# Kernel optimization log

Hardware: AMD Instinct MI355X
Metric: run time of the kernel (lower is better)

The kernel has to match this reference:

```python
import math
import jax, jax.numpy as jnp
import numpy as np

FACTOR = 2  # init kwarg of AutoCorrelation


def setup_inputs() -> dict:
    key0 = jax.random.key(0)
    kq, kk, kv = jax.random.split(key0, 3)
    B, H, L, D = 8, 8, 2048, 64
    return {
        "query": jax.random.normal(kq, (B, H, L, D), dtype=jnp.float32),
        "key": jax.random.normal(kk, (B, H, L, D), dtype=jnp.float32),
        "value": jax.random.normal(kv, (B, H, L, D), dtype=jnp.float32),
    }


def reference(query, key, value):
    # Inference (eval-mode) path of AutoCorrelation.forward.
    B, H, L, D = query.shape
    L_KV = key.shape[2]
    # _pad_or_truncate_key_value: match key/value length to query length
    if L > L_KV:
        pad = [(0, 0), (0, 0), (0, L - L_KV), (0, 0)]
        key = jnp.pad(key, pad)
        value = jnp.pad(value, pad)
    else:
        key = key[:, :, :L, :]
        value = value[:, :, :L, :]

    # _period_based_dependency: circular cross-correlation via FFT
    qf = jnp.fft.rfft(jnp.swapaxes(query, -2, -1), axis=-1)   # (B,H,D,L//2+1) complex
    kf = jnp.fft.rfft(jnp.swapaxes(key, -2, -1), axis=-1)
    corr = jnp.fft.irfft(qf * jnp.conj(kf), n=L, axis=-1)     # (B,H,D,L)

    # _time_delay_aggregation (eval branch: per-batch topk delays)
    mean_corr = corr.mean(axis=(1, 2))                         # (B,L)
    num_delays = min(FACTOR * math.ceil(math.log(L)), L)
    w, delay_idx = jax.lax.top_k(mean_corr, num_delays)       # (B,k)
    w = jax.nn.softmax(w, axis=-1)

    ar = jnp.arange(L)

    def body(ctx, inp):
        d, wk = inp  # (B,), (B,)
        idx = (ar[None, :] + d[:, None]) % L                   # (B,L) — circular shift == gather from doubled value
        gathered = jnp.take_along_axis(
            value, jnp.broadcast_to(idx[:, None, :, None], value.shape), axis=2
        )                                                      # (B,H,L,D)
        return ctx + wk[:, None, None, None] * gathered, None

    ctx0 = jnp.zeros_like(value)
    context, _ = jax.lax.scan(body, ctx0, (delay_idx.T, w.T))
    return context
```

## Files before the change

### kernel.cpp

```cpp
#include <hip/hip_runtime.h>

static constexpr int LSEQ = 2048;
static constexpr int NB   = 8;
static constexpr int NH   = 8;
static constexpr int ND   = 64;
static constexpr int NDEL = 16;

static constexpr size_t WS_P_OFF     = 0;
static constexpr size_t WS_S_OFF     = 8388608;
static constexpr size_t WS_W_OFF     = 8519680;
static constexpr size_t WS_DELAY_OFF = 8520192;

__device__ __forceinline__ int SW2(int j) { return j ^ ((j >> 4) & 15); }

__global__ __launch_bounds__(256) void fft_corr(const float* __restrict__ q,
                                                const float* __restrict__ k,
                                                float2* __restrict__ P) {
    __shared__ float2 z[4][LSEQ];
    __shared__ float2 tw[680];

    const int tid = threadIdx.x;
    const int bi  = blockIdx.x;
    const int xcd = bi & 7;
    const int sl  = bi >> 3;
    const int bh  = xcd * 8 + (sl >> 3);
    const int grp = sl & 7;
    const int b   = bh >> 3;
    const int h   = bh & 7;
    const size_t base = (size_t)bh * LSEQ * ND + (size_t)(grp * 8);

    for (int i = tid; i < 680; i += 256) {
        int idx, M;
        if (i < 512)      { idx = i;       M = 2048; }
        else if (i < 640) { idx = i - 512; M = 512; }
        else if (i < 672) { idx = i - 640; M = 128; }
        else              { idx = i - 672; M = 32; }
        float sn, cs;
        __sincosf(-6.28318530717958647692f * (float)idx / (float)M, &sn, &cs);
        tw[i] = make_float2(cs, sn);
    }

    float4 qa[8], ka[8];
    #pragma unroll
    for (int u = 0; u < 8; ++u) {
        const size_t r = base + (size_t)(tid + 256 * u) * ND;
        qa[u] = *(const float4*)(q + r);
        ka[u] = *(const float4*)(k + r);
    }
    #pragma unroll
    for (int u = 0; u < 8; ++u) {
        const int t = tid + 256 * u;
        #pragma unroll
        for (int c = 0; c < 4; ++c)
            z[c][SW2(t)] = make_float2((&qa[u].x)[c], (&ka[u].x)[c]);
    }
    float4 qb[8], kb[8];
    #pragma unroll
    for (int u = 0; u < 8; ++u) {
        const size_t r = base + (size_t)(tid + 256 * u) * ND + 4;
        qb[u] = *(const float4*)(q + r);
        kb[u] = *(const float4*)(k + r);
    }

    float accR[8], accI[8];
    #pragma unroll
    for (int u = 0; u < 8; ++u) { accR[u] = 0.f; accI[u] = 0.f; }

    const int lane = tid & 63;
    const int wch  = tid >> 6;
    const float RH = 0.70710678118654752440f;

    for (int round = 0; round < 2; ++round) {
        __syncthreads();

        const int tb[4] = {0, 512, 640, 672};
        #pragma unroll
        for (int st = 0; st < 4; ++st) {
            const int lq = 9 - 2 * st;
            const int qq = 1 << lq;
            const float2* twb = &tw[tb[st]];
            #pragma unroll
            for (int u = 0; u < 8; ++u) {
                const int j  = lane + (u << 6);
                const int kk = j & (qq - 1);
                const int i0 = ((j >> lq) << (lq + 2)) | kk;
                const float2 x0 = z[wch][SW2(i0)];
                const float2 x1 = z[wch][SW2(i0 + qq)];
                const float2 x2 = z[wch][SW2(i0 + 2 * qq)];
                const float2 x3 = z[wch][SW2(i0 + 3 * qq)];
                const float2 w1 = twb[kk];
                const float cs = w1.x, sn = w1.y;
                const float c2 = cs * cs - sn * sn, s2 = 2.f * cs * sn;
                const float Ar = x0.x + x2.x, Ai = x0.y + x2.y;
                const float B0r = x0.x - x2.x, B0i = x0.y - x2.y;
                const float Cr = x1.x + x3.x, Ci = x1.y + x3.y;
                const float D0r = x1.x - x3.x, D0i = x1.y - x3.y;
                z[wch][SW2(i0)] = make_float2(Ar + Cr, Ai + Ci);
                const float T1r = Ar - Cr, T1i = Ai - Ci;
                z[wch][SW2(i0 + qq)] =
                    make_float2(T1r * c2 - T1i * s2, T1r * s2 + T1i * c2);
                const float Br = B0r * cs - B0i * sn, Bi = B0r * sn + B0i * cs;
                const float Dr = D0r * sn + D0i * cs, Di = D0i * sn - D0r * cs;
                z[wch][SW2(i0 + 2 * qq)] = make_float2(Br + Dr, Bi + Di);
                const float T3r = Br - Dr, T3i = Bi - Di;
                z[wch][SW2(i0 + 3 * qq)] =
                    make_float2(T3r * c2 - T3i * s2, T3r * s2 + T3i * c2);
            }
            __syncthreads();
        }

        #pragma unroll
        for (int c4 = 0; c4 < 4; ++c4) {
            const int pb = tid << 3;
            float2 e[8];
            #pragma unroll
            for (int c = 0; c < 8; ++c) e[c] = z[c4][SW2(pb | c)];
            float ur[4], ui[4], vr[4], vi[4];
            ur[0] = e[0].x + e[4].x; ui[0] = e[0].y + e[4].y;
            vr[0] = e[0].x - e[4].x; vi[0] = e[0].y - e[4].y;
            { const float a = e[1].x - e[5].x, bq = e[1].y - e[5].y;
              ur[1] = e[1].x + e[5].x; ui[1] = e[1].y + e[5].y;
              vr[1] = RH * (a + bq); vi[1] = RH * (bq - a); }
            { const float a = e[2].x - e[6].x, bq = e[2].y - e[6].y;
              ur[2] = e[2].x + e[6].x; ui[2] = e[2].y + e[6].y;
              vr[2] = bq; vi[2] = -a; }
            { const float a = e[3].x - e[7].x, bq = e[3].y - e[7].y;
              ur[3] = e[3].x + e[7].x; ui[3] = e[3].y + e[7].y;
              vr[3] = RH * (bq - a); vi[3] = -RH * (a + bq); }
            {
                const float a0r = ur[0] + ur[2], a0i = ui[0] + ui[2];
                const float a2r = ur[0] - ur[2], a2i = ui[0] - ui[2];
                const float a1r = ur[1] + ur[3], a1i = ui[1] + ui[3];
                const float a3r = ui[1] - ui[3], a3i = -(ur[1] - ur[3]);
                z[c4][SW2(pb | 0)] = make_float2(a0r + a1r, a0i + a1i);
                z[c4][SW2(pb | 1)] = make_float2(a0r - a1r, a0i - a1i);
                z[c4][SW2(pb | 2)] = make_float2(a2r + a3r, a2i + a3i);
                z[c4][SW2(pb | 3)] = make_float2(a2r - a3r, a2i - a3i);
            }
            {
                const float a0r = vr[0] + vr[2], a0i = vi[0] + vi[2];
                const float a2r = vr[0] - vr[2], a2i = vi[0] - vi[2];
                const float a1r = vr[1] + vr[3], a1i = vi[1] + vi[3];
                const float a3r = vi[1] - vi[3], a3i = -(vr[1] - vr[3]);
                z[c4][SW2(pb | 4)] = make_float2(a0r + a1r, a0i + a1i);
                z[c4][SW2(pb | 5)] = make_float2(a0r - a1r, a0i - a1i);
                z[c4][SW2(pb | 6)] = make_float2(a2r + a3r, a2i + a3i);
                z[c4][SW2(pb | 7)] = make_float2(a2r - a3r, a2i - a3i);
            }
        }
        __syncthreads();

        #pragma unroll
        for (int u = 0; u < 8; ++u) {
            const int fb = wch * 8 + u;
            const int f  = fb | (lane << 5);
            const int m  = (2048 - f) & 2047;
            const int p  = (int)(__brev((unsigned)f) >> 21);
            const int pm = (int)(__brev((unsigned)m) >> 21);
            float sr = 0.f, si = 0.f;
            #pragma unroll
            for (int c = 0; c < 4; ++c) {
                const float2 Zf = z[c][SW2(p)];
                const float2 Zm = z[c][SW2(pm)];
                const float qr = 0.5f * (Zf.x + Zm.x), qi = 0.5f * (Zf.y - Zm.y);
                const float kr = 0.5f * (Zf.y + Zm.y), ki = 0.5f * (Zm.x - Zf.x);
                sr += qr * kr + qi * ki;
                si += qi * kr - qr * ki;
            }
            accR[u] += sr; accI[u] += si;
        }

        if (round == 0) {
            __syncthreads();
            #pragma unroll
            for (int u = 0; u < 8; ++u) {
                const int t = tid + 256 * u;
                #pragma unroll
                for (int c = 0; c < 4; ++c)
                    z[c][SW2(t)] = make_float2((&qb[u].x)[c], (&kb[u].x)[c]);
            }
        }
    }

    const int part = h * 8 + grp;
    float2* Pp = P + (size_t)part * (NB * 2048) + (size_t)b * 2048;
    #pragma unroll
    for (int u = 0; u < 8; ++u) {
        const int f = (wch * 8 + u) | (lane << 5);
        const int p = (int)(__brev((unsigned)f) >> 21);
        Pp[p] = make_float2(accR[u], accI[u]);
    }
}

__global__ __launch_bounds__(256) void reduce_S(const float2* __restrict__ P,
                                                float2* __restrict__ S) {
    const int g = blockIdx.x * 256 + threadIdx.x;
    float accx = 0.f, accy = 0.f;
    #pragma unroll 8
    for (int part = 0; part < 64; ++part) {
        const float2 v = P[(size_t)part * (NB * 2048) + g];
        accx += v.x; accy += v.y;
    }
    S[g] = make_float2(accx, accy);
}

__global__ __launch_bounds__(1024) void ifft_topk(const float2* __restrict__ S,
                                                  float* __restrict__ wout,
                                                  int* __restrict__ dout) {
    const int b = blockIdx.x, tid = threadIdx.x;
    __shared__ float2 y[LSEQ];
    __shared__ float  mc[LSEQ];
    __shared__ float  pv[16];
    __shared__ int    pi[16];
    __shared__ float  topv[NDEL];
    __shared__ int    topi[NDEL];

    y[tid]        = S[b * 2048 + tid];
    y[tid + 1024] = S[b * 2048 + tid + 1024];
    __syncthreads();

    for (int M = 2; M <= LSEQ; M <<= 1) {
        const int   half = M >> 1;
        const float w0   = 6.28318530717958647692f / (float)M;
        const int   kk = tid & (half - 1), i0 = 2 * tid - kk, i1 = i0 + half;
        const float2 a = y[i0], bb = y[i1];
        float sn, cs;
        __sincosf(w0 * (float)kk, &sn, &cs);
        const float tx = bb.x * cs - bb.y * sn, ty = bb.x * sn + bb.y * cs;
        y[i0] = make_float2(a.x + tx, a.y + ty);
        y[i1] = make_float2(a.x - tx, a.y - ty);
        __syncthreads();
    }

    const float scale = 1.0f / ((float)LSEQ * (float)(NH * ND));
    mc[tid]        = y[tid].x * scale;
    mc[tid + 1024] = y[tid + 1024].x * scale;
    __syncthreads();

    const int lane = tid & 63, wv = tid >> 6;
    for (int it = 0; it < NDEL; ++it) {
        const float v0 = mc[tid], v1 = mc[tid + 1024];
        float bv; int bix;
        if (v1 > v0) { bv = v1; bix = tid + 1024; } else { bv = v0; bix = tid; }
        #pragma unroll
        for (int off = 32; off; off >>= 1) {
            const float ov = __shfl_xor(bv, off);
            const int   oi = __shfl_xor(bix, off);
            if (ov > bv || (ov == bv && oi < bix)) { bv = ov; bix = oi; }
        }
        if (lane == 0) { pv[wv] = bv; pi[wv] = bix; }
        __syncthreads();
        if (tid < 64) {
            float v = (tid < 16) ? pv[tid] : -3e38f;
            int  ii = (tid < 16) ? pi[tid] : 0;
            #pragma unroll
            for (int off = 8; off; off >>= 1) {
                const float ov = __shfl_xor(v, off);
                const int   oi = __shfl_xor(ii, off);
                if (ov > v || (ov == v && oi < ii)) { v = ov; ii = oi; }
            }
            if (tid == 0) { topv[it] = v; topi[it] = ii; mc[ii] = -3e38f; }
        }
        __syncthreads();
    }

    if (tid == 0) {
        const float m = topv[0];
        float e[NDEL], sum = 0.f;
        for (int t2 = 0; t2 < NDEL; ++t2) { e[t2] = __expf(topv[t2] - m); sum += e[t2]; }
        const float inv = 1.0f / sum;
        for (int t2 = 0; t2 < NDEL; ++t2) {
            wout[b * NDEL + t2] = e[t2] * inv;
            dout[b * NDEL + t2] = topi[t2];
        }
    }
}

__global__ __launch_bounds__(256) void gather_out(const float* __restrict__ v,
                                                  const float* __restrict__ w,
                                                  const int* __restrict__ delay,
                                                  float* __restrict__ out) {
    const int bi  = blockIdx.x;
    const int xcd = bi & 7;
    const int s   = bi >> 3;
    const int bh  = xcd * 8 + (s >> 7);
    const int bt  = s & 127;
    const int b   = bh >> 3;
    const int tid = threadIdx.x;

    __shared__ float sw_[NDEL];
    __shared__ int   sd_[NDEL];
    if (tid < NDEL) {
        sw_[tid] = w[b * NDEL + tid];
        sd_[tid] = delay[b * NDEL + tid];
    }
    __syncthreads();

    const float* vb = v + (size_t)bh * LSEQ * ND;
    float*       ob = out + (size_t)bh * LSEQ * ND;

    const int row = tid >> 4;
    const int col = (tid & 15) * 4;
    const int t   = bt * 16 + row;

    float4 acc = make_float4(0.f, 0.f, 0.f, 0.f);
    #pragma unroll
    for (int kk = 0; kk < NDEL; ++kk) {
        const int r = (t + sd_[kk]) & (LSEQ - 1);
        const float4 vv = *(const float4*)(vb + (size_t)r * ND + col);
        const float wv = sw_[kk];
        acc.x += wv * vv.x; acc.y += wv * vv.y;
        acc.z += wv * vv.z; acc.w += wv * vv.w;
    }
    *(float4*)(ob + (size_t)t * ND + col) = acc;
}

extern "C" void kernel_launch(void* const* d_in, const int* in_sizes, int n_in,
                              void* d_out, int out_size, void* d_ws, size_t ws_size,
                              hipStream_t stream) {
    const float* q = (const float*)d_in[0];
    const float* k = (const float*)d_in[1];
    const float* v = (const float*)d_in[2];
    float* out = (float*)d_out;

    float2* P     = (float2*)((char*)d_ws + WS_P_OFF);
    float2* S     = (float2*)((char*)d_ws + WS_S_OFF);
    float*  w     = (float*)((char*)d_ws + WS_W_OFF);
    int*    delay = (int*)((char*)d_ws + WS_DELAY_OFF);

    fft_corr<<<dim3(512), dim3(256), 0, stream>>>(q, k, P);
    reduce_S<<<dim3(64), dim3(256), 0, stream>>>(P, S);
    ifft_topk<<<dim3(NB), dim3(1024), 0, stream>>>(S, w, delay);
    gather_out<<<dim3(NB * NH * 128), dim3(256), 0, stream>>>(v, w, delay, out);
}
```

Before: 226.9 us.

## Restructure FFT as radix-8 Stockham with register twiddles and fuse reduction into ifft

Replaces the four-column shared-memory radix-4 FFT with a single-column radix-8x8x8x4 decomposition that holds twiddles in registers and keeps the first pass in registers from global loads. Hermitian symmetry is used so each thread computes only half the spectrum bins and writes the conjugate mirrors. The separate reduce_S kernel is removed and its 64-way partial sum is folded into ifft_topk, saving one launch and one global round trip. In exchange there are more barriers per column, only 8 blocks do the reduction, and the index permutation logic is more complex.

```diff
diff --git a/kernel.cpp b/kernel.cpp
--- a/kernel.cpp
+++ b/kernel.cpp
@@ -7,19 +7,67 @@
 static constexpr int NDEL = 16;
 
 static constexpr size_t WS_P_OFF     = 0;
-static constexpr size_t WS_S_OFF     = 8388608;
-static constexpr size_t WS_W_OFF     = 8519680;
-static constexpr size_t WS_DELAY_OFF = 8520192;
-
-__device__ __forceinline__ int SW2(int j) { return j ^ ((j >> 4) & 15); }
-
-__global__ __launch_bounds__(256) void fft_corr(const float* __restrict__ q,
-                                                const float* __restrict__ k,
-                                                float2* __restrict__ P) {
-    __shared__ float2 z[4][LSEQ];
-    __shared__ float2 tw[680];
-
-    const int tid = threadIdx.x;
+static constexpr size_t WS_W_OFF     = 8388608;
+static constexpr size_t WS_DELAY_OFF = 8389120;
+
+__device__ __forceinline__ int SWZ(int x) { return x ^ (((x >> 4) & 7) << 1); }
+
+__device__ __forceinline__ int pof(int f) {
+    return ((f & 7) << 8) | (((f >> 3) & 7) << 5) | (((f >> 6) & 7) << 2) | (f >> 9);
+}
+__device__ __forceinline__ int fofp(int p) {
+    return (p >> 8) | (((p >> 5) & 7) << 3) | (((p >> 2) & 7) << 6) | ((p & 3) << 9);
+}
+
+#define CMUL(ar, ai, br, bi) make_float2((ar)*(br) - (ai)*(bi), (ar)*(bi) + (ai)*(br))
+
+__device__ __forceinline__ void dft8(const float2 x[8], float2 X[8]) {
+    const float RH = 0.70710678118654752440f;
+    float2 a0 = make_float2(x[0].x + x[4].x, x[0].y + x[4].y);
+    float2 a1 = make_float2(x[1].x + x[5].x, x[1].y + x[5].y);
+    float2 a2 = make_float2(x[2].x + x[6].x, x[2].y + x[6].y);
+    float2 a3 = make_float2(x[3].x + x[7].x, x[3].y + x[7].y);
+    float2 b0 = make_float2(x[0].x - x[4].x, x[0].y - x[4].y);
+    float  t1r = x[1].x - x[5].x, t1i = x[1].y - x[5].y;
+    float2 b1 = make_float2(RH * (t1r + t1i), RH * (t1i - t1r));
+    float  t2r = x[2].x - x[6].x, t2i = x[2].y - x[6].y;
+    float2 b2 = make_float2(t2i, -t2r);
+    float  t3r = x[3].x - x[7].x, t3i = x[3].y - x[7].y;
+    float2 b3 = make_float2(RH * (t3i - t3r), -RH * (t3r + t3i));
+    float2 c0 = make_float2(a0.x + a2.x, a0.y + a2.y);
+    float2 d0 = make_float2(a0.x - a2.x, a0.y - a2.y);
+    float2 c1 = make_float2(a1.x + a3.x, a1.y + a3.y);
+    float2 d1 = make_float2(a1.y - a3.y, -(a1.x - a3.x));
+    X[0] = make_float2(c0.x + c1.x, c0.y + c1.y);
+    X[4] = make_float2(c0.x - c1.x, c0.y - c1.y);
+    X[2] = make_float2(d0.x + d1.x, d0.y + d1.y);
+    X[6] = make_float2(d0.x - d1.x, d0.y - d1.y);
+    float2 e0 = make_float2(b0.x + b2.x, b0.y + b2.y);
+    float2 f0 = make_float2(b0.x - b2.x, b0.y - b2.y);
+    float2 e1 = make_float2(b1.x + b3.x, b1.y + b3.y);
+    float2 f1 = make_float2(b1.y - b3.y, -(b1.x - b3.x));
+    X[1] = make_float2(e0.x + e1.x, e0.y + e1.y);
+    X[5] = make_float2(e0.x - e1.x, e0.y - e1.y);
+    X[3] = make_float2(f0.x + f1.x, f0.y + f1.y);
+    X[7] = make_float2(f0.x - f1.x, f0.y - f1.y);
+}
+
+__device__ __forceinline__ void dft4(const float2 x[4], float2 X[4]) {
+    float2 s0 = make_float2(x[0].x + x[2].x, x[0].y + x[2].y);
+    float2 s1 = make_float2(x[1].x + x[3].x, x[1].y + x[3].y);
+    float2 d0 = make_float2(x[0].x - x[2].x, x[0].y - x[2].y);
+    float2 d1 = make_float2(x[1].y - x[3].y, -(x[1].x - x[3].x));
+    X[0] = make_float2(s0.x + s1.x, s0.y + s1.y);
+    X[2] = make_float2(s0.x - s1.x, s0.y - s1.y);
+    X[1] = make_float2(d0.x + d1.x, d0.y + d1.y);
+    X[3] = make_float2(d0.x - d1.x, d0.y - d1.y);
+}
+
+__global__ __launch_bounds__(256, 3) void fft_corr(const float* __restrict__ q,
+                                                   const float* __restrict__ k,
+                                                   float2* __restrict__ P) {
+    __shared__ float2 z[LSEQ];
+    const int t   = threadIdx.x;
     const int bi  = blockIdx.x;
     const int xcd = bi & 7;
     const int sl  = bi >> 3;
@@ -29,182 +77,131 @@
     const int h   = bh & 7;
     const size_t base = (size_t)bh * LSEQ * ND + (size_t)(grp * 8);
 
-    for (int i = tid; i < 680; i += 256) {
-        int idx, M;
-        if (i < 512)      { idx = i;       M = 2048; }
-        else if (i < 640) { idx = i - 512; M = 512; }
-        else if (i < 672) { idx = i - 640; M = 128; }
-        else              { idx = i - 672; M = 32; }
+    float2 WA[7], WB[7], WC[7];
+    {
         float sn, cs;
-        __sincosf(-6.28318530717958647692f * (float)idx / (float)M, &sn, &cs);
-        tw[i] = make_float2(cs, sn);
-    }
-
-    float4 qa[8], ka[8];
+        __sincosf(-6.28318530717958647692f * (float)t / 2048.f, &sn, &cs);
+        WA[0] = make_float2(cs, sn);
+        __sincosf(-6.28318530717958647692f * (float)(t & 31) / 256.f, &sn, &cs);
+        WB[0] = make_float2(cs, sn);
+        __sincosf(-6.28318530717958647692f * (float)(t & 3) / 32.f, &sn, &cs);
+        WC[0] = make_float2(cs, sn);
+        #pragma unroll
+        for (int m = 1; m < 7; ++m) {
+            WA[m] = CMUL(WA[m-1].x, WA[m-1].y, WA[0].x, WA[0].y);
+            WB[m] = CMUL(WB[m-1].x, WB[m-1].y, WB[0].x, WB[0].y);
+            WC[m] = CMUL(WC[m-1].x, WC[m-1].y, WC[0].x, WC[0].y);
+        }
+    }
+
+    int fS[4], pmS[4];
     #pragma unroll
-    for (int u = 0; u < 8; ++u) {
-        const size_t r = base + (size_t)(tid + 256 * u) * ND;
-        qa[u] = *(const float4*)(q + r);
-        ka[u] = *(const float4*)(k + r);
-    }
-    #pragma unroll
-    for (int u = 0; u < 8; ++u) {
-        const int t = tid + 256 * u;
+    for (int s = 0; s < 4; ++s) {
+        const int cc = (s < 2) ? s : s + 2;
+        const int f  = fofp(8 * t + cc);
+        const int m  = (2048 - f) & 2047;
+        fS[s]  = f;
+        pmS[s] = SWZ(pof(m));
+    }
+    float aFr[4] = {0, 0, 0, 0}, aFi[4] = {0, 0, 0, 0};
+    float aS = 0.f;
+
+    const int sbB   = (t >> 5) * 256 + (t & 31);
+    const int baseC = (t >> 2) * 32 + (t & 3);
+
+    for (int half = 0; half < 2; ++half) {
+        float4 qa[8], ka[8];
         #pragma unroll
-        for (int c = 0; c < 4; ++c)
-            z[c][SW2(t)] = make_float2((&qa[u].x)[c], (&ka[u].x)[c]);
-    }
-    float4 qb[8], kb[8];
-    #pragma unroll
-    for (int u = 0; u < 8; ++u) {
-        const size_t r = base + (size_t)(tid + 256 * u) * ND + 4;
-        qb[u] = *(const float4*)(q + r);
-        kb[u] = *(const float4*)(k + r);
-    }
-
-    float accR[8], accI[8];
-    #pragma unroll
-    for (int u = 0; u < 8; ++u) { accR[u] = 0.f; accI[u] = 0.f; }
-
-    const int lane = tid & 63;
-    const int wch  = tid >> 6;
-    const float RH = 0.70710678118654752440f;
-
-    for (int round = 0; round < 2; ++round) {
-        __syncthreads();
-
-        const int tb[4] = {0, 512, 640, 672};
+        for (int j = 0; j < 8; ++j) {
+            const size_t r = base + (size_t)(t + 256 * j) * ND + half * 4;
+            qa[j] = *(const float4*)(q + r);
+            ka[j] = *(const float4*)(k + r);
+        }
         #pragma unroll
-        for (int st = 0; st < 4; ++st) {
-            const int lq = 9 - 2 * st;
-            const int qq = 1 << lq;
-            const float2* twb = &tw[tb[st]];
-            #pragma unroll
-            for (int u = 0; u < 8; ++u) {
-                const int j  = lane + (u << 6);
-                const int kk = j & (qq - 1);
-                const int i0 = ((j >> lq) << (lq + 2)) | kk;
-                const float2 x0 = z[wch][SW2(i0)];
-                const float2 x1 = z[wch][SW2(i0 + qq)];
-                const float2 x2 = z[wch][SW2(i0 + 2 * qq)];
-                const float2 x3 = z[wch][SW2(i0 + 3 * qq)];
-                const float2 w1 = twb[kk];
-                const float cs = w1.x, sn = w1.y;
-                const float c2 = cs * cs - sn * sn, s2 = 2.f * cs * sn;
-                const float Ar = x0.x + x2.x, Ai = x0.y + x2.y;
-                const float B0r = x0.x - x2.x, B0i = x0.y - x2.y;
-                const float Cr = x1.x + x3.x, Ci = x1.y + x3.y;
-                const float D0r = x1.x - x3.x, D0i = x1.y - x3.y;
-                z[wch][SW2(i0)] = make_float2(Ar + Cr, Ai + Ci);
-                const float T1r = Ar - Cr, T1i = Ai - Ci;
-                z[wch][SW2(i0 + qq)] =
-                    make_float2(T1r * c2 - T1i * s2, T1r * s2 + T1i * c2);
-                const float Br = B0r * cs - B0i * sn, Bi = B0r * sn + B0i * cs;
-                const float Dr = D0r * sn + D0i * cs, Di = D0i * sn - D0r * cs;
-                z[wch][SW2(i0 + 2 * qq)] = make_float2(Br + Dr, Bi + Di);
-                const float T3r = Br - Dr, T3i = Bi - Di;
-                z[wch][SW2(i0 + 3 * qq)] =
-                    make_float2(T3r * c2 - T3i * s2, T3r * s2 + T3i * c2);
-            }
-            __syncthreads();
-        }
-
-        #pragma unroll
-        for (int c4 = 0; c4 < 4; ++c4) {
-            const int pb = tid << 3;
-            float2 e[8];
-            #pragma unroll
-            for (int c = 0; c < 8; ++c) e[c] = z[c4][SW2(pb | c)];
-            float ur[4], ui[4], vr[4], vi[4];
-            ur[0] = e[0].x + e[4].x; ui[0] = e[0].y + e[4].y;
-            vr[0] = e[0].x - e[4].x; vi[0] = e[0].y - e[4].y;
-            { const float a = e[1].x - e[5].x, bq = e[1].y - e[5].y;
-              ur[1] = e[1].x + e[5].x; ui[1] = e[1].y + e[5].y;
-              vr[1] = RH * (a + bq); vi[1] = RH * (bq - a); }
-            { const float a = e[2].x - e[6].x, bq = e[2].y - e[6].y;
-              ur[2] = e[2].x + e[6].x; ui[2] = e[2].y + e[6].y;
-              vr[2] = bq; vi[2] = -a; }
-            { const float a = e[3].x - e[7].x, bq = e[3].y - e[7].y;
-              ur[3] = e[3].x + e[7].x; ui[3] = e[3].y + e[7].y;
-              vr[3] = RH * (bq - a); vi[3] = -RH * (a + bq); }
+        for (int c = 0; c < 4; ++c) {
+            float2 X[8], Y[8];
+            #pragma unroll
+            for (int j = 0; j < 8; ++j)
+                X[j] = make_float2((&qa[j].x)[c], (&ka[j].x)[c]);
+
+            __syncthreads();
+
+            dft8(X, Y);
+            #pragma unroll
+            for (int m = 1; m < 8; ++m) Y[m] = CMUL(Y[m].x, Y[m].y, WA[m-1].x, WA[m-1].y);
+            #pragma unroll
+            for (int m = 0; m < 8; ++m) z[SWZ(m * 256 + t)] = Y[m];
+            __syncthreads();
+
             {
-                const float a0r = ur[0] + ur[2], a0i = ui[0] + ui[2];
-                const float a2r = ur[0] - ur[2], a2i = ui[0] - ui[2];
-                const float a1r = ur[1] + ur[3], a1i = ui[1] + ui[3];
-                const float a3r = ui[1] - ui[3], a3i = -(ur[1] - ur[3]);
-                z[c4][SW2(pb | 0)] = make_float2(a0r + a1r, a0i + a1i);
-                z[c4][SW2(pb | 1)] = make_float2(a0r - a1r, a0i - a1i);
-                z[c4][SW2(pb | 2)] = make_float2(a2r + a3r, a2i + a3i);
-                z[c4][SW2(pb | 3)] = make_float2(a2r - a3r, a2i - a3i);
-            }
+                int adr[8];
+                #pragma unroll
+                for (int n = 0; n < 8; ++n) adr[n] = SWZ(sbB + 32 * n);
+                #pragma unroll
+                for (int j = 0; j < 8; ++j) X[j] = z[adr[j]];
+                dft8(X, Y);
+                #pragma unroll
+                for (int m = 1; m < 8; ++m) Y[m] = CMUL(Y[m].x, Y[m].y, WB[m-1].x, WB[m-1].y);
+                #pragma unroll
+                for (int m = 0; m < 8; ++m) z[adr[m]] = Y[m];
+            }
+            __syncthreads();
+
             {
-                const float a0r = vr[0] + vr[2], a0i = vi[0] + vi[2];
-                const float a2r = vr[0] - vr[2], a2i = vi[0] - vi[2];
-                const float a1r = vr[1] + vr[3], a1i = vi[1] + vi[3];
-                const float a3r = vi[1] - vi[3], a3i = -(vr[1] - vr[3]);
-                z[c4][SW2(pb | 4)] = make_float2(a0r + a1r, a0i + a1i);
-                z[c4][SW2(pb | 5)] = make_float2(a0r - a1r, a0i - a1i);
-                z[c4][SW2(pb | 6)] = make_float2(a2r + a3r, a2i + a3i);
-                z[c4][SW2(pb | 7)] = make_float2(a2r - a3r, a2i - a3i);
-            }
-        }
-        __syncthreads();
-
-        #pragma unroll
-        for (int u = 0; u < 8; ++u) {
-            const int fb = wch * 8 + u;
-            const int f  = fb | (lane << 5);
-            const int m  = (2048 - f) & 2047;
-            const int p  = (int)(__brev((unsigned)f) >> 21);
-            const int pm = (int)(__brev((unsigned)m) >> 21);
-            float sr = 0.f, si = 0.f;
-            #pragma unroll
-            for (int c = 0; c < 4; ++c) {
-                const float2 Zf = z[c][SW2(p)];
-                const float2 Zm = z[c][SW2(pm)];
+                int adr[8];
+                #pragma unroll
+                for (int n = 0; n < 8; ++n) adr[n] = SWZ(baseC + 4 * n);
+                #pragma unroll
+                for (int j = 0; j < 8; ++j) X[j] = z[adr[j]];
+                dft8(X, Y);
+                #pragma unroll
+                for (int m = 1; m < 8; ++m) Y[m] = CMUL(Y[m].x, Y[m].y, WC[m-1].x, WC[m-1].y);
+                #pragma unroll
+                for (int m = 0; m < 8; ++m) z[adr[m]] = Y[m];
+            }
+            __syncthreads();
+
+            {
+                int adr[8];
+                #pragma unroll
+                for (int n = 0; n < 8; ++n) adr[n] = SWZ(8 * t + n);
+                float2 xin[8];
+                #pragma unroll
+                for (int j = 0; j < 8; ++j) xin[j] = z[adr[j]];
+                dft4(&xin[0], &X[0]);
+                dft4(&xin[4], &X[4]);
+                #pragma unroll
+                for (int m = 0; m < 8; ++m) z[adr[m]] = X[m];
+            }
+            __syncthreads();
+
+            #pragma unroll
+            for (int s = 0; s < 4; ++s) {
+                const int cc = (s < 2) ? s : s + 2;
+                const float2 Zf = X[cc];
+                const float2 Zm = z[pmS[s]];
                 const float qr = 0.5f * (Zf.x + Zm.x), qi = 0.5f * (Zf.y - Zm.y);
                 const float kr = 0.5f * (Zf.y + Zm.y), ki = 0.5f * (Zm.x - Zf.x);
-                sr += qr * kr + qi * ki;
-                si += qi * kr - qr * ki;
-            }
-            accR[u] += sr; accI[u] += si;
-        }
-
-        if (round == 0) {
-            __syncthreads();
-            #pragma unroll
-            for (int u = 0; u < 8; ++u) {
-                const int t = tid + 256 * u;
-                #pragma unroll
-                for (int c = 0; c < 4; ++c)
-                    z[c][SW2(t)] = make_float2((&qb[u].x)[c], (&kb[u].x)[c]);
-            }
+                aFr[s] += qr * kr + qi * ki;
+                aFi[s] += qi * kr - qr * ki;
+            }
+            if (t == 0) aS += X[2].x * X[2].y;
         }
     }
 
     const int part = h * 8 + grp;
     float2* Pp = P + (size_t)part * (NB * 2048) + (size_t)b * 2048;
+    *(float4*)&Pp[8 * t]     = make_float4(aFr[0], aFi[0], aFr[1], aFi[1]);
+    *(float4*)&Pp[8 * t + 4] = make_float4(aFr[2], aFi[2], aFr[3], aFi[3]);
     #pragma unroll
-    for (int u = 0; u < 8; ++u) {
-        const int f = (wch * 8 + u) | (lane << 5);
-        const int p = (int)(__brev((unsigned)f) >> 21);
-        Pp[p] = make_float2(accR[u], accI[u]);
-    }
-}
-
-__global__ __launch_bounds__(256) void reduce_S(const float2* __restrict__ P,
-                                                float2* __restrict__ S) {
-    const int g = blockIdx.x * 256 + threadIdx.x;
-    float accx = 0.f, accy = 0.f;
-    #pragma unroll 8
-    for (int part = 0; part < 64; ++part) {
-        const float2 v = P[(size_t)part * (NB * 2048) + g];
-        accx += v.x; accy += v.y;
-    }
-    S[g] = make_float2(accx, accy);
-}
-
-__global__ __launch_bounds__(1024) void ifft_topk(const float2* __restrict__ S,
+    for (int s = 0; s < 4; ++s) {
+        const int m = (2048 - fS[s]) & 2047;
+        if (m != fS[s]) Pp[pof(m)] = make_float2(aFr[s], -aFi[s]);
+    }
+    if (t == 0) Pp[pof(1024)] = make_float2(aS, 0.f);
+}
+
+__global__ __launch_bounds__(1024) void ifft_topk(const float2* __restrict__ P,
                                                   float* __restrict__ wout,
                                                   int* __restrict__ dout) {
     const int b = blockIdx.x, tid = threadIdx.x;
@@ -215,8 +212,16 @@
     __shared__ float  topv[NDEL];
     __shared__ int    topi[NDEL];
 
-    y[tid]        = S[b * 2048 + tid];
-    y[tid + 1024] = S[b * 2048 + tid + 1024];
+    float2 s0 = make_float2(0.f, 0.f), s1 = make_float2(0.f, 0.f);
+    const float2* Pb = P + (size_t)b * 2048;
+    #pragma unroll 8
+    for (int part = 0; part < 64; ++part) {
+        const float2 v0 = Pb[(size_t)part * (NB * 2048) + tid];
+        const float2 v1 = Pb[(size_t)part * (NB * 2048) + tid + 1024];
+        s0.x += v0.x; s0.y += v0.y; s1.x += v1.x; s1.y += v1.y;
+    }
+    y[__brev((unsigned)fofp(tid)) >> 21]        = s0;
+    y[__brev((unsigned)fofp(tid + 1024)) >> 21] = s1;
     __syncthreads();
 
     for (int M = 2; M <= LSEQ; M <<= 1) {
@@ -324,12 +329,10 @@
     float* out = (float*)d_out;
 
     float2* P     = (float2*)((char*)d_ws + WS_P_OFF);
-    float2* S     = (float2*)((char*)d_ws + WS_S_OFF);
     float*  w     = (float*)((char*)d_ws + WS_W_OFF);
     int*    delay = (int*)((char*)d_ws + WS_DELAY_OFF);
 
     fft_corr<<<dim3(512), dim3(256), 0, stream>>>(q, k, P);
-    reduce_S<<<dim3(64), dim3(256), 0, stream>>>(P, S);
-    ifft_topk<<<dim3(NB), dim3(1024), 0, stream>>>(S, w, delay);
+    ifft_topk<<<dim3(NB), dim3(1024), 0, stream>>>(P, w, delay);
     gather_out<<<dim3(NB * NH * 128), dim3(256), 0, stream>>>(v, w, delay, out);
 }
```

After: 226.7 us. About the same (-0.1%).
